# Performance work log

Hardware: AMD Instinct MI355X
Metric: run time of the kernel (lower is better)

Reference implementation:

```python
import jax, jax.numpy as jnp
import numpy as np
import math

INPUT_DIM = 1024
OUTPUT_DIM = 8192
M_BLOCKS = 8  # ceil(OUTPUT_DIM / INPUT_DIM)
SCALE = 1.0


def fwht(x):
    """Unnormalized fast Walsh-Hadamard transform over the last axis.
    Matches the torch recursive-cat implementation (Sylvester/natural order).
    """
    n = x.shape[-1]
    lead = x.shape[:-1]
    h = 1
    while h < n:
        y = x.reshape(lead + (n // (2 * h), 2, h))
        a = y[..., 0, :]
        b = y[..., 1, :]
        x = jnp.stack([a + b, a - b], axis=-2).reshape(lead + (n,))
        h *= 2
    return x


def setup_inputs() -> dict:
    key = jax.random.key(0)
    kx, kb, kg, ks, kp, ku = jax.random.split(key, 6)
    x = jax.random.normal(kx, (8, 1024, INPUT_DIM), dtype=jnp.float32)
    B = jax.random.normal(kb, (M_BLOCKS, INPUT_DIM), dtype=jnp.float32)
    G = jax.random.normal(kg, (M_BLOCKS, INPUT_DIM), dtype=jnp.float32)
    S = jax.random.uniform(ks, (M_BLOCKS, INPUT_DIM), dtype=jnp.float32)
    P = jax.random.randint(kp, (M_BLOCKS, INPUT_DIM), 0, INPUT_DIM, dtype=jnp.int64)
    u_rand = jax.random.uniform(ku, (OUTPUT_DIM,), dtype=jnp.float32)
    return {"x": x, "B": B, "G": G, "S": S, "P": P, "u_rand": u_rand}


def reference(x, B, G, S, P, u_rand):
    d = INPUT_DIM
    # flatten all leading dims into rows: (R, 1, d)
    xr = x.reshape(-1, 1, d)
    Bx = xr * B                                   # (R, m, d)
    HBx = fwht(Bx)                                # (R, m, d)
    idx = jnp.broadcast_to(P[None], HBx.shape)    # per-block permutation gather
    PHBx = jnp.take_along_axis(HBx, idx, axis=-1)
    GPHBx = PHBx * G
    HGPHBx = fwht(GPHBx)
    SHGPHBx = HGPHBx * S
    norm_factor = 1.0 / (SCALE * math.sqrt(d))
    Vx = norm_factor * SHGPHBx.reshape(SHGPHBx.shape[0], -1)  # (R, m*d)
    result = Vx[:, :OUTPUT_DIM]
    # phi nonlinearity: cos(x + 2*pi*U) * sqrt(2/output_dim)
    phase = (2.0 * jnp.pi) * u_rand
    result = jnp.cos(result + phase) * math.sqrt(2.0 / OUTPUT_DIM)
    return result
```

## Files before the change

kernel.cpp:

```cpp
#include <hip/hip_runtime.h>
#include <math.h>


template <int CTRL>
__device__ __forceinline__ float dpp_f(float x) {
    return __int_as_float(
        __builtin_amdgcn_mov_dpp(__float_as_int(x), CTRL, 0xF, 0xF, true));
}

#define DPP_XOR1 0xB1
#define DPP_XOR2 0x4E
#define DPP_XOR3 0x1B
#define DPP_HMIR 0x141
#define DPP_ROR8 0x128

__device__ __forceinline__ void fwht_phaseA(float v[16], float sg0, float sg1,
                                            float sg2, float sg3) {
#pragma unroll
    for (int h = 1; h < 16; h <<= 1) {
#pragma unroll
        for (int k = 0; k < 16; ++k) {
            if (!(k & h)) {
                float a = v[k], b = v[k ^ h];
                v[k] = a + b;
                v[k ^ h] = a - b;
            }
        }
    }
#pragma unroll
    for (int k = 0; k < 16; ++k) v[k] = fmaf(v[k], sg0, dpp_f<DPP_XOR1>(v[k]));
#pragma unroll
    for (int k = 0; k < 16; ++k) v[k] = fmaf(v[k], sg1, dpp_f<DPP_XOR2>(v[k]));
#pragma unroll
    for (int k = 0; k < 16; ++k)
        v[k] = fmaf(v[k], sg2, dpp_f<DPP_XOR3>(dpp_f<DPP_HMIR>(v[k])));
#pragma unroll
    for (int k = 0; k < 16; ++k) v[k] = fmaf(v[k], sg3, dpp_f<DPP_ROR8>(v[k]));
}

__device__ __forceinline__ void fwht_phaseB(float v[16]) {
#pragma unroll
    for (int k = 0; k < 16; ++k) {
        if (!(k & 4)) { float a = v[k], b = v[k ^ 4]; v[k] = a + b; v[k ^ 4] = a - b; }
    }
#pragma unroll
    for (int k = 0; k < 16; ++k) {
        if (!(k & 8)) { float a = v[k], b = v[k ^ 8]; v[k] = a + b; v[k ^ 8] = a - b; }
    }
}

__global__ __launch_bounds__(256) void fastfood_kernel(
    const float* __restrict__ x, const float* __restrict__ B,
    const float* __restrict__ G, const float* __restrict__ S,
    const int* __restrict__ P, const float* __restrict__ u_rand,
    float* __restrict__ out)
{
    __shared__ float lds[4 * 1088];
    const int lane = threadIdx.x & 63;
    const int wv   = threadIdx.x >> 6;
    const int row  = blockIdx.x * 4 + wv;

    const float sg0 = (lane & 1) ? -1.f : 1.f;
    const float sg1 = (lane & 2) ? -1.f : 1.f;
    const float sg2 = (lane & 4) ? -1.f : 1.f;
    const float sg3 = (lane & 8) ? -1.f : 1.f;

    float* wlds = lds + wv * 1088;
    float4* w4L1 = (float4*)(wlds + 16 * lane + 4 * (lane >> 2));
    int addrL2[4];
#pragma unroll
    for (int b = 0; b < 4; ++b) {
        int i0 = b * 256 + 4 * lane;
        addrL2[b] = i0 + 4 * (i0 >> 6);
    }

    const float c_arg = 0.03125f * 0.15915494309189535f;
    const float c_amp = 0.015625f;

    float xv[16];
    {
        const float4* x4 = (const float4*)(x + (size_t)row * 1024 + 16 * lane);
#pragma unroll
        for (int j = 0; j < 4; ++j) {
            float4 t = x4[j];
            xv[4 * j + 0] = t.x; xv[4 * j + 1] = t.y;
            xv[4 * j + 2] = t.z; xv[4 * j + 3] = t.w;
        }
    }

#pragma unroll 1
    for (int m = 0; m < 8; ++m) {
        const int mo = m * 1024;
        float v[16];

        {
            const float4* B4 = (const float4*)(B + mo + 16 * lane);
#pragma unroll
            for (int j = 0; j < 4; ++j) {
                float4 b = B4[j];
                v[4 * j + 0] = xv[4 * j + 0] * b.x;
                v[4 * j + 1] = xv[4 * j + 1] * b.y;
                v[4 * j + 2] = xv[4 * j + 2] * b.z;
                v[4 * j + 3] = xv[4 * j + 3] * b.w;
            }
        }

        fwht_phaseA(v, sg0, sg1, sg2, sg3);
#pragma unroll
        for (int j = 0; j < 4; ++j)
            w4L1[j] = make_float4(v[4 * j + 0], v[4 * j + 1], v[4 * j + 2], v[4 * j + 3]);
#pragma unroll
        for (int b = 0; b < 4; ++b) {
            float4 t = *(const float4*)(wlds + addrL2[b]);
            v[4 * b + 0] = t.x; v[4 * b + 1] = t.y;
            v[4 * b + 2] = t.z; v[4 * b + 3] = t.w;
        }
        fwht_phaseB(v);

#pragma unroll
        for (int b = 0; b < 4; ++b)
            *(float4*)(wlds + addrL2[b]) =
                make_float4(v[4 * b + 0], v[4 * b + 1], v[4 * b + 2], v[4 * b + 3]);

        {
            const int4*   P4 = (const int4*)(P + mo + 16 * lane);
            const float4* G4 = (const float4*)(G + mo + 16 * lane);
#pragma unroll
            for (int j = 0; j < 4; ++j) {
                int4 p = P4[j];
                float4 g = G4[j];
                v[4 * j + 0] = wlds[p.x + ((p.x >> 6) << 2)] * g.x;
                v[4 * j + 1] = wlds[p.y + ((p.y >> 6) << 2)] * g.y;
                v[4 * j + 2] = wlds[p.z + ((p.z >> 6) << 2)] * g.z;
                v[4 * j + 3] = wlds[p.w + ((p.w >> 6) << 2)] * g.w;
            }
        }

        fwht_phaseA(v, sg0, sg1, sg2, sg3);
#pragma unroll
        for (int j = 0; j < 4; ++j)
            w4L1[j] = make_float4(v[4 * j + 0], v[4 * j + 1], v[4 * j + 2], v[4 * j + 3]);
#pragma unroll
        for (int b = 0; b < 4; ++b) {
            float4 t = *(const float4*)(wlds + addrL2[b]);
            v[4 * b + 0] = t.x; v[4 * b + 1] = t.y;
            v[4 * b + 2] = t.z; v[4 * b + 3] = t.w;
        }
        fwht_phaseB(v);

        {
            const float4* S4 = (const float4*)(S + mo);
            const float4* U4 = (const float4*)(u_rand + mo);
            float4* o4 = (float4*)(out + (size_t)row * 8192 + mo);
#pragma unroll
            for (int b = 0; b < 4; ++b) {
                int idx = b * 64 + lane;
                float4 sv = S4[idx], uv = U4[idx], rr;
                rr.x = __builtin_amdgcn_cosf(__builtin_amdgcn_fractf(
                           fmaf(v[4 * b + 0] * sv.x, c_arg, uv.x))) * c_amp;
                rr.y = __builtin_amdgcn_cosf(__builtin_amdgcn_fractf(
                           fmaf(v[4 * b + 1] * sv.y, c_arg, uv.y))) * c_amp;
                rr.z = __builtin_amdgcn_cosf(__builtin_amdgcn_fractf(
                           fmaf(v[4 * b + 2] * sv.z, c_arg, uv.z))) * c_amp;
                rr.w = __builtin_amdgcn_cosf(__builtin_amdgcn_fractf(
                           fmaf(v[4 * b + 3] * sv.w, c_arg, uv.w))) * c_amp;
                o4[idx] = rr;
            }
        }
    }
}

extern "C" void kernel_launch(void* const* d_in, const int* in_sizes, int n_in,
                              void* d_out, int out_size, void* d_ws, size_t ws_size,
                              hipStream_t stream) {
    const float* x = (const float*)d_in[0];
    const float* B = (const float*)d_in[1];
    const float* G = (const float*)d_in[2];
    const float* S = (const float*)d_in[3];
    const int*   P = (const int*)d_in[4];
    const float* u = (const float*)d_in[5];
    float* out = (float*)d_out;

    dim3 grid(2048), block(256);
    hipLaunchKernelGGL(fastfood_kernel, grid, block, 0, stream,
                       x, B, G, S, P, u, out);
}
```

Measured before the change: 368.3 us.

## Finish FWHT in registers via cross-lane permutes, drop LDS transpose passes

Replaces the LDS transpose plus in-register butterfly stages with permlane16/permlane32 swaps (falling back to ds_swizzle/shfl_xor), so both Hadamard transforms complete without staging through shared memory. The output then ends up in a different index layout, so the gather uses P and G loaded with a strided-by-lane pattern and the final stores use a matching layout. It also adds nontemporal loads for x and nontemporal stores for the output. The risk is correctness of the new layout mapping, and the cost of the cross-lane ops versus the LDS traffic they replace.

```diff
diff --git a/kernel.cpp b/kernel.cpp
--- a/kernel.cpp
+++ b/kernel.cpp
@@ -1,6 +1,9 @@
 #include <hip/hip_runtime.h>
 #include <math.h>
 
+
+typedef unsigned uint2_ev __attribute__((ext_vector_type(2)));
+typedef float    f32x4    __attribute__((ext_vector_type(4)));
 
 template <int CTRL>
 __device__ __forceinline__ float dpp_f(float x) {
@@ -14,8 +17,10 @@
 #define DPP_HMIR 0x141
 #define DPP_ROR8 0x128
 
-__device__ __forceinline__ void fwht_phaseA(float v[16], float sg0, float sg1,
-                                            float sg2, float sg3) {
+__device__ __forceinline__ void fwht_full(float v[16], float sg0, float sg1,
+                                          float sg2, float sg3, float sg4,
+                                          float sg5) {
+    (void)sg4; (void)sg5;
 #pragma unroll
     for (int h = 1; h < 16; h <<= 1) {
 #pragma unroll
@@ -36,17 +41,49 @@
         v[k] = fmaf(v[k], sg2, dpp_f<DPP_XOR3>(dpp_f<DPP_HMIR>(v[k])));
 #pragma unroll
     for (int k = 0; k < 16; ++k) v[k] = fmaf(v[k], sg3, dpp_f<DPP_ROR8>(v[k]));
-}
-
-__device__ __forceinline__ void fwht_phaseB(float v[16]) {
+
+#if __has_builtin(__builtin_amdgcn_permlane16_swap)
+#pragma unroll
+    for (int p = 0; p < 8; ++p) {
+        uint2_ev r = __builtin_amdgcn_permlane16_swap(
+            __float_as_uint(v[2 * p]), __float_as_uint(v[2 * p + 1]), false,
+            false);
+        float s = __uint_as_float(r.x) + __uint_as_float(r.y);
+        float d = __uint_as_float(r.x) - __uint_as_float(r.y);
+        uint2_ev q = __builtin_amdgcn_permlane16_swap(
+            __float_as_uint(s), __float_as_uint(d), false, false);
+        v[2 * p]     = __uint_as_float(q.x);
+        v[2 * p + 1] = __uint_as_float(q.y);
+    }
+#else
 #pragma unroll
     for (int k = 0; k < 16; ++k) {
-        if (!(k & 4)) { float a = v[k], b = v[k ^ 4]; v[k] = a + b; v[k ^ 4] = a - b; }
-    }
+        float t = __int_as_float(
+            __builtin_amdgcn_ds_swizzle(__float_as_int(v[k]), 0x401F));
+        v[k] = fmaf(v[k], sg4, t);
+    }
+#endif
+
+#if __has_builtin(__builtin_amdgcn_permlane32_swap)
+#pragma unroll
+    for (int p = 0; p < 8; ++p) {
+        uint2_ev r = __builtin_amdgcn_permlane32_swap(
+            __float_as_uint(v[2 * p]), __float_as_uint(v[2 * p + 1]), false,
+            false);
+        float s = __uint_as_float(r.x) + __uint_as_float(r.y);
+        float d = __uint_as_float(r.x) - __uint_as_float(r.y);
+        uint2_ev q = __builtin_amdgcn_permlane32_swap(
+            __float_as_uint(s), __float_as_uint(d), false, false);
+        v[2 * p]     = __uint_as_float(q.x);
+        v[2 * p + 1] = __uint_as_float(q.y);
+    }
+#else
 #pragma unroll
     for (int k = 0; k < 16; ++k) {
-        if (!(k & 8)) { float a = v[k], b = v[k ^ 8]; v[k] = a + b; v[k ^ 8] = a - b; }
-    }
+        float t = __shfl_xor(v[k], 32, 64);
+        v[k] = fmaf(v[k], sg5, t);
+    }
+#endif
 }
 
 __global__ __launch_bounds__(256) void fastfood_kernel(
@@ -60,29 +97,26 @@
     const int wv   = threadIdx.x >> 6;
     const int row  = blockIdx.x * 4 + wv;
 
-    const float sg0 = (lane & 1) ? -1.f : 1.f;
-    const float sg1 = (lane & 2) ? -1.f : 1.f;
-    const float sg2 = (lane & 4) ? -1.f : 1.f;
-    const float sg3 = (lane & 8) ? -1.f : 1.f;
+    const float sg0 = (lane & 1)  ? -1.f : 1.f;
+    const float sg1 = (lane & 2)  ? -1.f : 1.f;
+    const float sg2 = (lane & 4)  ? -1.f : 1.f;
+    const float sg3 = (lane & 8)  ? -1.f : 1.f;
+    const float sg4 = (lane & 16) ? -1.f : 1.f;
+    const float sg5 = (lane & 32) ? -1.f : 1.f;
 
     float* wlds = lds + wv * 1088;
     float4* w4L1 = (float4*)(wlds + 16 * lane + 4 * (lane >> 2));
-    int addrL2[4];
-#pragma unroll
-    for (int b = 0; b < 4; ++b) {
-        int i0 = b * 256 + 4 * lane;
-        addrL2[b] = i0 + 4 * (i0 >> 6);
-    }
 
     const float c_arg = 0.03125f * 0.15915494309189535f;
     const float c_amp = 0.015625f;
 
     float xv[16];
     {
-        const float4* x4 = (const float4*)(x + (size_t)row * 1024 + 16 * lane);
+        const f32x4* x4 =
+            (const f32x4*)(x + (size_t)row * 1024 + 16 * lane);
 #pragma unroll
         for (int j = 0; j < 4; ++j) {
-            float4 t = x4[j];
+            f32x4 t = __builtin_nontemporal_load(&x4[j]);
             xv[4 * j + 0] = t.x; xv[4 * j + 1] = t.y;
             xv[4 * j + 2] = t.z; xv[4 * j + 3] = t.w;
         }
@@ -105,57 +139,44 @@
             }
         }
 
-        fwht_phaseA(v, sg0, sg1, sg2, sg3);
+        fwht_full(v, sg0, sg1, sg2, sg3, sg4, sg5);
+
+        const int4*   P4 = (const int4*)(P + mo);
+        const float4* G4 = (const float4*)(G + mo);
+        int4   pj[4];
+        float4 gj[4];
+#pragma unroll
+        for (int j = 0; j < 4; ++j) {
+            pj[j] = P4[64 * j + lane];
+            gj[j] = G4[64 * j + lane];
+        }
+
 #pragma unroll
         for (int j = 0; j < 4; ++j)
-            w4L1[j] = make_float4(v[4 * j + 0], v[4 * j + 1], v[4 * j + 2], v[4 * j + 3]);
-#pragma unroll
-        for (int b = 0; b < 4; ++b) {
-            float4 t = *(const float4*)(wlds + addrL2[b]);
-            v[4 * b + 0] = t.x; v[4 * b + 1] = t.y;
-            v[4 * b + 2] = t.z; v[4 * b + 3] = t.w;
-        }
-        fwht_phaseB(v);
-
-#pragma unroll
-        for (int b = 0; b < 4; ++b)
-            *(float4*)(wlds + addrL2[b]) =
-                make_float4(v[4 * b + 0], v[4 * b + 1], v[4 * b + 2], v[4 * b + 3]);
-
-        {
-            const int4*   P4 = (const int4*)(P + mo + 16 * lane);
-            const float4* G4 = (const float4*)(G + mo + 16 * lane);
-#pragma unroll
-            for (int j = 0; j < 4; ++j) {
-                int4 p = P4[j];
-                float4 g = G4[j];
-                v[4 * j + 0] = wlds[p.x + ((p.x >> 6) << 2)] * g.x;
-                v[4 * j + 1] = wlds[p.y + ((p.y >> 6) << 2)] * g.y;
-                v[4 * j + 2] = wlds[p.z + ((p.z >> 6) << 2)] * g.z;
-                v[4 * j + 3] = wlds[p.w + ((p.w >> 6) << 2)] * g.w;
-            }
-        }
-
-        fwht_phaseA(v, sg0, sg1, sg2, sg3);
-#pragma unroll
-        for (int j = 0; j < 4; ++j)
-            w4L1[j] = make_float4(v[4 * j + 0], v[4 * j + 1], v[4 * j + 2], v[4 * j + 3]);
-#pragma unroll
-        for (int b = 0; b < 4; ++b) {
-            float4 t = *(const float4*)(wlds + addrL2[b]);
-            v[4 * b + 0] = t.x; v[4 * b + 1] = t.y;
-            v[4 * b + 2] = t.z; v[4 * b + 3] = t.w;
-        }
-        fwht_phaseB(v);
+            w4L1[j] = make_float4(v[4 * j + 0], v[4 * j + 1],
+                                  v[4 * j + 2], v[4 * j + 3]);
+
+#pragma unroll
+        for (int j = 0; j < 4; ++j) {
+            int4 p = pj[j];
+            float4 g = gj[j];
+            v[4 * j + 0] = wlds[p.x + ((p.x >> 6) << 2)] * g.x;
+            v[4 * j + 1] = wlds[p.y + ((p.y >> 6) << 2)] * g.y;
+            v[4 * j + 2] = wlds[p.z + ((p.z >> 6) << 2)] * g.z;
+            v[4 * j + 3] = wlds[p.w + ((p.w >> 6) << 2)] * g.w;
+        }
+
+        fwht_full(v, sg0, sg1, sg2, sg3, sg4, sg5);
 
         {
             const float4* S4 = (const float4*)(S + mo);
             const float4* U4 = (const float4*)(u_rand + mo);
-            float4* o4 = (float4*)(out + (size_t)row * 8192 + mo);
+            f32x4* o4 = (f32x4*)(out + (size_t)row * 8192 + mo);
 #pragma unroll
             for (int b = 0; b < 4; ++b) {
                 int idx = b * 64 + lane;
-                float4 sv = S4[idx], uv = U4[idx], rr;
+                float4 sv = S4[idx], uv = U4[idx];
+                f32x4 rr;
                 rr.x = __builtin_amdgcn_cosf(__builtin_amdgcn_fractf(
                            fmaf(v[4 * b + 0] * sv.x, c_arg, uv.x))) * c_amp;
                 rr.y = __builtin_amdgcn_cosf(__builtin_amdgcn_fractf(
@@ -164,7 +185,7 @@
                            fmaf(v[4 * b + 2] * sv.z, c_arg, uv.z))) * c_amp;
                 rr.w = __builtin_amdgcn_cosf(__builtin_amdgcn_fractf(
                            fmaf(v[4 * b + 3] * sv.w, c_arg, uv.w))) * c_amp;
-                o4[idx] = rr;
+                __builtin_nontemporal_store(rr, &o4[idx]);
             }
         }
     }
```

Measured after the change: 345.3 us. 6.2% less time.
